# Optimization experiments

Hardware: AMD Instinct MI355X
Metric: run time of the kernel (lower is better)

Reference implementation:

```python
import jax, jax.numpy as jnp
import numpy as np

EMBED_DIM = 512
NUM_HEADS = 8
WINDOW = 64
FFN_RATIO = 4


def _mha(q_in, kv_in, w_in, b_in, w_out, b_out, n_heads, mask=None):
    # Faithful torch.nn.MultiheadAttention (batch_first) with packed in_proj.
    b, sq, d = q_in.shape
    sk = kv_in.shape[1]
    hd = d // n_heads
    wq, wk, wv = jnp.split(w_in, 3, axis=0)   # each [d, d]
    bq, bk, bv = jnp.split(b_in, 3, axis=0)
    q = (q_in @ wq.T + bq).reshape(b, sq, n_heads, hd).transpose(0, 2, 1, 3)
    k = (kv_in @ wk.T + bk).reshape(b, sk, n_heads, hd).transpose(0, 2, 1, 3)
    v = (kv_in @ wv.T + bv).reshape(b, sk, n_heads, hd).transpose(0, 2, 1, 3)
    scores = jnp.einsum('bhqd,bhkd->bhqk', q, k) / jnp.sqrt(jnp.asarray(hd, q.dtype))
    if mask is not None:
        scores = scores + mask  # additive -inf mask, broadcast over [b, h]
    attn = jax.nn.softmax(scores, axis=-1)
    out = jnp.einsum('bhqk,bhkd->bhqd', attn, v)
    out = out.transpose(0, 2, 1, 3).reshape(b, sq, d)
    return out @ w_out.T + b_out


def _layernorm(x, g, b, eps=1e-5):
    mu = jnp.mean(x, axis=-1, keepdims=True)
    var = jnp.var(x, axis=-1, keepdims=True)
    return (x - mu) * jax.lax.rsqrt(var + eps) * g + b


def _local_causal_mask(p, window, dtype=jnp.float32):
    # row i attends to columns [max(0, i-window), i]
    i = jnp.arange(p)[:, None]
    j = jnp.arange(p)[None, :]
    allowed = (j <= i) & (j >= i - window)
    return jnp.where(allowed, jnp.zeros((), dtype), jnp.asarray(-jnp.inf, dtype))


def setup_inputs() -> dict:
    key = jax.random.key(0)
    ks = jax.random.split(key, 20)
    d, h = EMBED_DIM, EMBED_DIM * FFN_RATIO
    s = 0.02
    return {
        'x': jax.random.normal(ks[0], (64, 512, d), jnp.float32),
        'anchors': jax.random.normal(ks[1], (64, 32, d), jnp.float32),
        'lw_in': jax.random.normal(ks[2], (3 * d, d), jnp.float32) * s,
        'lb_in': jnp.zeros((3 * d,), jnp.float32),
        'lw_out': jax.random.normal(ks[3], (d, d), jnp.float32) * s,
        'lb_out': jnp.zeros((d,), jnp.float32),
        'gw_in': jax.random.normal(ks[4], (3 * d, d), jnp.float32) * s,
        'gb_in': jnp.zeros((3 * d,), jnp.float32),
        'gw_out': jax.random.normal(ks[5], (d, d), jnp.float32) * s,
        'gb_out': jnp.zeros((d,), jnp.float32),
        'w1': jax.random.normal(ks[6], (h, d), jnp.float32) * s,
        'b1': jnp.zeros((h,), jnp.float32),
        'w2': jax.random.normal(ks[7], (d, h), jnp.float32) * s,
        'b2': jnp.zeros((d,), jnp.float32),
        'g1': jnp.ones((d,), jnp.float32),
        'be1': jnp.zeros((d,), jnp.float32),
        'g2': jnp.ones((d,), jnp.float32),
        'be2': jnp.zeros((d,), jnp.float32),
    }


def reference(x, anchors, lw_in, lb_in, lw_out, lb_out, gw_in, gb_in, gw_out, gb_out,
              w1, b1, w2, b2, g1, be1, g2, be2):
    p = x.shape[1]
    mask = _local_causal_mask(p, WINDOW, x.dtype)
    x = x + _mha(x, x, lw_in, lb_in, lw_out, lb_out, NUM_HEADS, mask)
    x = x + _mha(x, anchors, gw_in, gb_in, gw_out, gb_out, NUM_HEADS)
    x = _layernorm(x, g1, be1)
    h = jax.nn.gelu(x @ w1.T + b1, approximate=False)
    ffn = h @ w2.T + b2
    return _layernorm(x + ffn, g2, be2)
```

## Files before the change

### kernel.cpp

```cpp
#include <hip/hip_runtime.h>
#include <cmath>


typedef unsigned short u16;
typedef unsigned int u32;
typedef __bf16 bf16_t;
typedef bf16_t bf16x8 __attribute__((ext_vector_type(8)));
typedef float f32x4 __attribute__((ext_vector_type(4)));

#define DEV __device__ __forceinline__
#define MFMA16(a, b, c) __builtin_amdgcn_mfma_f32_16x16x32_bf16(a, b, c, 0, 0, 0)
#define SBAR() __builtin_amdgcn_sched_barrier(0)

DEV u16 f2b(float f) {
  u32 u = __float_as_uint(f);
  u32 r = u + 0x7fffu + ((u >> 16) & 1u);
  return (u16)(r >> 16);
}
DEV float b2f(u16 b) { return __uint_as_float(((u32)b) << 16); }

DEV float gelu_erf(float x) {
  float y = x * 0.70710678118654752f;
  float ay = fabsf(y);
  float t = __builtin_amdgcn_rcpf(1.0f + 0.3275911f * ay);
  float p = t * (0.254829592f +
            t * (-0.284496736f +
            t * (1.421413741f +
            t * (-1.453152027f + t * 1.061405429f))));
  float e = 1.0f - p * __expf(-y * y);
  float erfv = (y < 0.f) ? -e : e;
  return 0.5f * x * (1.0f + erfv);
}

DEV void g2l16(const void* g, void* l) {
  __builtin_amdgcn_global_load_lds((const __attribute__((address_space(1))) void*)g,
                                   (__attribute__((address_space(3))) void*)l,
                                   16, 0, 0);
}

__global__ __launch_bounds__(256) void conv1(const float* __restrict__ s,
                                             u16* __restrict__ d) {
  size_t idx = ((size_t)blockIdx.x * 256 + threadIdx.x) * 8;
  float4 a = *(const float4*)(s + idx);
  float4 b = *(const float4*)(s + idx + 4);
  float v[8] = {a.x, a.y, a.z, a.w, b.x, b.y, b.z, b.w};
  union { u16 q[8]; uint4 u; } pk;
#pragma unroll
  for (int i = 0; i < 8; ++i) pk.q[i] = f2b(v[i]);
  *(uint4*)(d + idx) = pk.u;
}

template <bool GELU, bool RES32, bool RESB, bool LN, bool OUT32, bool OUTB>
__global__ __launch_bounds__(1024, 1) void gemmW(
    const u16* __restrict__ A, const u16* __restrict__ B,
    const float* __restrict__ bias, const float* __restrict__ res32,
    const u16* __restrict__ resb, const float* __restrict__ lnG,
    const float* __restrict__ lnB, float* __restrict__ out32,
    u16* __restrict__ outb, int M, int N, int K) {
  __shared__ __align__(16) char smem[147456];
  const int tid = threadIdx.x;
  const int lane = tid & 63, wv = tid >> 6;
  const int wm = wv >> 3, wn = wv & 7;
  const int lrow = lane & 15, quad = lane >> 4;

  int idx = blockIdx.x;
  {
    const int nwg = gridDim.x;
    if (nwg >= 8) {
      const int q = nwg >> 3, r = nwg & 7;
      const int xcd = idx & 7, rk = idx >> 3;
      idx = (xcd < r ? xcd * (q + 1) : r * (q + 1) + (xcd - r) * q) + rk;
    }
  }
  const int nx = N >> 9;
  const int m0 = (idx / nx) * 128, n0 = (idx % nx) * 512;

  const int c0q = quad ^ (lrow & 3);
  const int hbit = (lrow >> 2) & 1;
  int aOffE[4], aOffO[4], bOff[4];
#pragma unroll
  for (int m = 0; m < 4; ++m) {
    const int rb = (wm * 64 + m * 16 + lrow) * 128;
    aOffE[m] = rb + (c0q + hbit * 4) * 16;
    aOffO[m] = rb + (c0q + (1 - hbit) * 4) * 16;
  }
#pragma unroll
  for (int n = 0; n < 4; ++n)
    bOff[n] = (wn * 64 + n * 16 + lrow) * 64 + ((quad ^ ((lrow >> 1) & 3)) * 16);

  const int lB = (tid & 3) ^ ((tid >> 3) & 3);
  const char* Bsrc0 = (const char*)B + (((size_t)(n0 + (tid >> 2)) * K + lB * 8) << 1);
  const char* Bsrc1 = (const char*)B + (((size_t)(n0 + 256 + (tid >> 2)) * K + lB * 8) << 1);
  const int lA = (tid & 7) ^ ((tid >> 3) & 7);
  const char* Asrc = (const char*)A + (((size_t)(m0 + (tid >> 3)) * K + lA * 8) << 1);

  const int nt = K >> 5, ntp = nt >> 1;
  const int sdst = tid * 16;

  f32x4 acc[4][4];
  f32x4 zero4 = {0.f, 0.f, 0.f, 0.f};
#pragma unroll
  for (int a = 0; a < 4; ++a)
#pragma unroll
    for (int b = 0; b < 4; ++b) acc[a][b] = zero4;

  g2l16(Asrc, smem + sdst);
  g2l16(Asrc + 128, smem + 16384 + sdst);
  g2l16(Bsrc0, smem + 49152 + sdst);
  g2l16(Bsrc1, smem + 49152 + 16384 + sdst);
  g2l16(Bsrc0 + 64, smem + 49152 + 32768 + sdst);
  g2l16(Bsrc1 + 64, smem + 49152 + 32768 + 16384 + sdst);
  SBAR();
  asm volatile("s_waitcnt vmcnt(2)" ::: "memory");
  asm volatile("s_barrier" ::: "memory");
  SBAR();

  int sB0 = 0, sB2 = 2, pA = 0, pA2 = 2;
  for (int tp = 0; tp < ntp; ++tp) {
#pragma unroll
    for (int half = 0; half < 2; ++half) {
      const int t = tp * 2 + half;
      const char* Ab = smem + pA * 16384;
      const char* Bb = smem + 49152 + sB0 * 32768;
      bf16x8 afr[4], bfr[4];
#pragma unroll
      for (int m = 0; m < 4; ++m)
        afr[m] = *(const bf16x8*)(Ab + (half ? aOffO[m] : aOffE[m]));
#pragma unroll
      for (int n = 0; n < 4; ++n)
        bfr[n] = *(const bf16x8*)(Bb + bOff[n]);
      const int ktB = (t + 2 < nt) ? t + 2 : nt - 1;
      char* bd = smem + 49152 + sB2 * 32768;
      g2l16(Bsrc0 + ((size_t)ktB << 6), bd + sdst);
      g2l16(Bsrc1 + ((size_t)ktB << 6), bd + 16384 + sdst);
      if (half == 0) {
        const int p2 = (tp + 2 < ntp) ? tp + 2 : ntp - 1;
        g2l16(Asrc + ((size_t)p2 << 7), smem + pA2 * 16384 + sdst);
      }
      SBAR();
      asm volatile("s_waitcnt lgkmcnt(0)" ::: "memory");
      SBAR();
      __builtin_amdgcn_s_setprio(1);
#pragma unroll
      for (int m = 0; m < 4; ++m)
#pragma unroll
        for (int n = 0; n < 4; ++n)
          acc[m][n] = MFMA16(afr[m], bfr[n], acc[m][n]);
      __builtin_amdgcn_s_setprio(0);
      SBAR();
      asm volatile("s_waitcnt vmcnt(3)" ::: "memory");
      asm volatile("s_barrier" ::: "memory");
      SBAR();
      sB0 = (sB0 == 2) ? 0 : sB0 + 1;
      sB2 = (sB2 == 2) ? 0 : sB2 + 1;
    }
    pA = (pA == 2) ? 0 : pA + 1;
    pA2 = (pA2 == 2) ? 0 : pA2 + 1;
  }

  asm volatile("s_waitcnt vmcnt(0)" ::: "memory");
  __syncthreads();

  float* cw = (float*)(smem + (size_t)wv * 4352);
  float* red = (float*)(smem + 131072);
  const int row16 = lane >> 2;
  const int c0 = (lane & 3) * 16;
  const int gcb = n0 + wn * 64 + c0;
  float bias16[16];
#pragma unroll
  for (int t = 0; t < 4; ++t) {
    float4 b4 = *(const float4*)(bias + gcb + t * 4);
    bias16[t * 4 + 0] = b4.x; bias16[t * 4 + 1] = b4.y;
    bias16[t * 4 + 2] = b4.z; bias16[t * 4 + 3] = b4.w;
  }

  float vv[4][16];
#pragma unroll
  for (int fm = 0; fm < 4; ++fm) {
#pragma unroll
    for (int fn = 0; fn < 4; ++fn)
#pragma unroll
      for (int r = 0; r < 4; ++r)
        cw[(quad * 4 + r) * 68 + fn * 16 + lrow] = acc[fm][fn][r];
    const int grow = m0 + wm * 64 + fm * 16 + row16;
    const size_t gbase = (size_t)grow * N + gcb;
    const float* crp = &cw[row16 * 68 + c0];
    float v[16];
#pragma unroll
    for (int t = 0; t < 4; ++t) {
      f32x4 q = *(const f32x4*)(crp + t * 4);
      v[t * 4 + 0] = q[0] + bias16[t * 4 + 0];
      v[t * 4 + 1] = q[1] + bias16[t * 4 + 1];
      v[t * 4 + 2] = q[2] + bias16[t * 4 + 2];
      v[t * 4 + 3] = q[3] + bias16[t * 4 + 3];
    }
    if (RES32) {
#pragma unroll
      for (int t = 0; t < 4; ++t) {
        float4 rr = *(const float4*)(res32 + gbase + t * 4);
        v[t * 4 + 0] += rr.x; v[t * 4 + 1] += rr.y;
        v[t * 4 + 2] += rr.z; v[t * 4 + 3] += rr.w;
      }
    }
    if (RESB) {
#pragma unroll
      for (int t = 0; t < 2; ++t) {
        union { u16 q[8]; uint4 u; } rb;
        rb.u = *(const uint4*)(resb + gbase + t * 8);
#pragma unroll
        for (int j = 0; j < 8; ++j) v[t * 8 + j] += b2f(rb.q[j]);
      }
    }
    if (GELU) {
#pragma unroll
      for (int e = 0; e < 16; ++e) v[e] = gelu_erf(v[e]);
    }
    if (LN) {
      float s1 = 0.f, s2 = 0.f;
#pragma unroll
      for (int e = 0; e < 16; ++e) { s1 += v[e]; s2 += v[e] * v[e]; }
      s1 += __shfl_xor(s1, 1); s2 += __shfl_xor(s2, 1);
      s1 += __shfl_xor(s1, 2); s2 += __shfl_xor(s2, 2);
      if ((lane & 3) == 0) {
        const int lr = wm * 64 + fm * 16 + row16;
        red[(lr * 8 + wn) * 2 + 0] = s1;
        red[(lr * 8 + wn) * 2 + 1] = s2;
      }
#pragma unroll
      for (int e = 0; e < 16; ++e) vv[fm][e] = v[e];
    } else {
      if (OUT32) {
#pragma unroll
        for (int t = 0; t < 4; ++t) {
          float4 w4 = {v[t * 4 + 0], v[t * 4 + 1], v[t * 4 + 2], v[t * 4 + 3]};
          *(float4*)(out32 + gbase + t * 4) = w4;
        }
      }
      if (OUTB) {
#pragma unroll
        for (int t = 0; t < 2; ++t) {
          union { u16 q[8]; uint4 u; } pk;
#pragma unroll
          for (int j = 0; j < 8; ++j) pk.q[j] = f2b(v[t * 8 + j]);
          *(uint4*)(outb + gbase + t * 8) = pk.u;
        }
      }
    }
  }

  if (LN) {
    __syncthreads();
    float g16[16], b16[16];
#pragma unroll
    for (int t = 0; t < 4; ++t) {
      float4 gg = *(const float4*)(lnG + gcb + t * 4);
      float4 bb = *(const float4*)(lnB + gcb + t * 4);
      g16[t * 4 + 0] = gg.x; g16[t * 4 + 1] = gg.y;
      g16[t * 4 + 2] = gg.z; g16[t * 4 + 3] = gg.w;
      b16[t * 4 + 0] = bb.x; b16[t * 4 + 1] = bb.y;
      b16[t * 4 + 2] = bb.z; b16[t * 4 + 3] = bb.w;
    }
#pragma unroll
    for (int fm = 0; fm < 4; ++fm) {
      const int lr = wm * 64 + fm * 16 + row16;
      const float* rp = &red[lr * 16];
      float s1 = 0.f, s2 = 0.f;
#pragma unroll
      for (int t = 0; t < 4; ++t) {
        f32x4 q = *(const f32x4*)(rp + t * 4);
        s1 += q[0] + q[2];
        s2 += q[1] + q[3];
      }
      const float mean = s1 * (1.0f / 512.0f);
      const float var = s2 * (1.0f / 512.0f) - mean * mean;
      const float rs = rsqrtf(var + 1e-5f);
      const int grow = m0 + wm * 64 + fm * 16 + row16;
      const size_t gbase = (size_t)grow * N + gcb;
      float o[16];
#pragma unroll
      for (int e = 0; e < 16; ++e)
        o[e] = (vv[fm][e] - mean) * rs * g16[e] + b16[e];
      if (OUT32) {
#pragma unroll
        for (int t = 0; t < 4; ++t) {
          float4 w4 = {o[t * 4 + 0], o[t * 4 + 1], o[t * 4 + 2], o[t * 4 + 3]};
          *(float4*)(out32 + gbase + t * 4) = w4;
        }
      }
      if (OUTB) {
#pragma unroll
        for (int t = 0; t < 2; ++t) {
          union { u16 q[8]; uint4 u; } pk;
#pragma unroll
          for (int j = 0; j < 8; ++j) pk.q[j] = f2b(o[t * 8 + j]);
          *(uint4*)(outb + gbase + t * 8) = pk.u;
        }
      }
    }
  }
}

__global__ __launch_bounds__(256) void local_attn_mfma(const u16* __restrict__ qkv,
                                                       u16* __restrict__ outb) {
  __shared__ u16 vt[64][152];
  __shared__ u16 pb[4][16][104];
  const int tid = threadIdx.x;
  const int lane = tid & 63, w = tid >> 6;
  const int c = lane & 15, quad = lane >> 4;
  const int bx = blockIdx.x;
  const int qb = bx & 7, h = (bx >> 3) & 7, bb = bx >> 6;
  const int i0 = qb * 64;
  const int hc = h * 64;
  const size_t rbase = (size_t)bb * 512;

  {
    int r = tid >> 1;
    int d0 = (tid & 1) * 32;
    int key = i0 - 64 + r;
    if (key < 0) key = 0;
    if (key > 511) key = 511;
    const u16* Vr = qkv + (rbase + key) * 1536 + 1024 + hc + d0;
#pragma unroll
    for (int g = 0; g < 4; ++g) {
      union { u16 q[8]; uint4 u; } vv;
      vv.u = *(const uint4*)(Vr + g * 8);
#pragma unroll
      for (int j = 0; j < 8; ++j) vt[d0 + g * 8 + j][r] = vv.q[j];
    }
    if (tid < 128) {
      int r2 = 128 + (tid >> 3);
      int d2 = (tid & 7) * 8;
      int key2 = i0 - 64 + r2;
      if (key2 < 0) key2 = 0;
      if (key2 > 511) key2 = 511;
      const u16* Vr2 = qkv + (rbase + key2) * 1536 + 1024 + hc + d2;
      union { u16 q[8]; uint4 u; } vv2;
      vv2.u = *(const uint4*)Vr2;
#pragma unroll
      for (int j = 0; j < 8; ++j) vt[d2 + j][r2] = vv2.q[j];
    }
  }
  __syncthreads();

  const int i0w = i0 + 16 * w;
  const int kg0 = i0w - 64;

  bf16x8 qf0, qf1;
  {
    const u16* Qr = qkv + (rbase + i0w + c) * 1536 + hc + quad * 8;
    qf0 = *(const bf16x8*)Qr;
    qf1 = *(const bf16x8*)(Qr + 32);
  }

  f32x4 s[5];
#pragma unroll
  for (int kb = 0; kb < 5; ++kb) {
    int key = kg0 + kb * 16 + c; if (key < 0) key = 0;
    const u16* Kr = qkv + (rbase + key) * 1536 + 512 + hc + quad * 8;
    bf16x8 k0 = *(const bf16x8*)Kr;
    bf16x8 k1 = *(const bf16x8*)(Kr + 32);
    f32x4 z = {0.f, 0.f, 0.f, 0.f};
    z = __builtin_amdgcn_mfma_f32_16x16x32_bf16(qf0, k0, z, 0, 0, 0);
    s[kb] = __builtin_amdgcn_mfma_f32_16x16x32_bf16(qf1, k1, z, 0, 0, 0);
  }

  float mx[4];
#pragma unroll
  for (int r = 0; r < 4; ++r) {
    int row = quad * 4 + r;
    float m = -1e30f;
#pragma unroll
    for (int kb = 0; kb < 5; ++kb) {
      float v = s[kb][r] * 0.125f;
      int key = kg0 + kb * 16 + c;
      bool ok = key >= 0;
      if (kb == 0) ok = ok && (c >= row);
      if (kb == 4) ok = ok && (c <= row);
      v = ok ? v : -1e30f;
      s[kb][r] = v;
      m = fmaxf(m, v);
    }
    mx[r] = m;
  }
#pragma unroll
  for (int o = 1; o <= 8; o <<= 1)
#pragma unroll
    for (int r = 0; r < 4; ++r) mx[r] = fmaxf(mx[r], __shfl_xor(mx[r], o));

  float l[4] = {0.f, 0.f, 0.f, 0.f};
#pragma unroll
  for (int kb = 0; kb < 5; ++kb)
#pragma unroll
    for (int r = 0; r < 4; ++r) {
      u16 pq = f2b(__expf(s[kb][r] - mx[r]));
      l[r] += b2f(pq);
      pb[w][quad * 4 + r][kb * 16 + c] = pq;
    }
#pragma unroll
  for (int r = 0; r < 4; ++r) pb[w][quad * 4 + r][80 + c] = 0;
#pragma unroll
  for (int o = 1; o <= 8; o <<= 1)
#pragma unroll
    for (int r = 0; r < 4; ++r) l[r] += __shfl_xor(l[r], o);
  float inv[4];
#pragma unroll
  for (int r = 0; r < 4; ++r) inv[r] = 1.f / l[r];

  f32x4 o4[4];
#pragma unroll
  for (int nb = 0; nb < 4; ++nb) o4[nb] = f32x4{0.f, 0.f, 0.f, 0.f};
#pragma unroll
  for (int kt = 0; kt < 3; ++kt) {
    bf16x8 pa = *(const bf16x8*)&pb[w][c][kt * 32 + quad * 8];
#pragma unroll
    for (int nb = 0; nb < 4; ++nb) {
      bf16x8 vb = *(const bf16x8*)&vt[nb * 16 + c][16 * w + kt * 32 + quad * 8];
      o4[nb] = __builtin_amdgcn_mfma_f32_16x16x32_bf16(pa, vb, o4[nb], 0, 0, 0);
    }
  }
#pragma unroll
  for (int nb = 0; nb < 4; ++nb)
#pragma unroll
    for (int r = 0; r < 4; ++r) {
      int seq = i0w + quad * 4 + r;
      outb[(rbase + seq) * 512 + hc + nb * 16 + c] = f2b(o4[nb][r] * inv[r]);
    }
}

__global__ __launch_bounds__(256) void global_attn_mfma(const u16* __restrict__ qg,
                                                        const u16* __restrict__ kvg,
                                                        u16* __restrict__ outb) {
  __shared__ u16 vt[64][40];
  __shared__ u16 pb[4][16][40];
  const int tid = threadIdx.x;
  const int lane = tid & 63, w = tid >> 6;
  const int c = lane & 15, quad = lane >> 4;
  const int bx = blockIdx.x;
  const int qb = bx & 7, h = (bx >> 3) & 7, bb = bx >> 6;
  const int i0 = qb * 64;
  const int hc = h * 64;
  const size_t rbase = (size_t)bb * 512;

  {
    int r = tid >> 3;
    int d0 = (tid & 7) * 8;
    const u16* Vr = kvg + ((size_t)bb * 32 + r) * 1024 + 512 + hc + d0;
    union { u16 q[8]; uint4 u; } vv;
    vv.u = *(const uint4*)Vr;
#pragma unroll
    for (int j = 0; j < 8; ++j) vt[d0 + j][r] = vv.q[j];
  }
  __syncthreads();

  const int i0w = i0 + 16 * w;
  bf16x8 qf0, qf1;
  {
    const u16* Qr = qg + (rbase + i0w + c) * 512 + hc + quad * 8;
    qf0 = *(const bf16x8*)Qr;
    qf1 = *(const bf16x8*)(Qr + 32);
  }
  f32x4 s[2];
#pragma unroll
  for (int kb = 0; kb < 2; ++kb) {
    const u16* Kr = kvg + ((size_t)bb * 32 + kb * 16 + c) * 1024 + hc + quad * 8;
    bf16x8 k0 = *(const bf16x8*)Kr;
    bf16x8 k1 = *(const bf16x8*)(Kr + 32);
    f32x4 z = {0.f, 0.f, 0.f, 0.f};
    z = __builtin_amdgcn_mfma_f32_16x16x32_bf16(qf0, k0, z, 0, 0, 0);
    s[kb] = __builtin_amdgcn_mfma_f32_16x16x32_bf16(qf1, k1, z, 0, 0, 0);
  }
  float mx[4];
#pragma unroll
  for (int r = 0; r < 4; ++r)
    mx[r] = fmaxf(s[0][r] * 0.125f, s[1][r] * 0.125f);
#pragma unroll
  for (int o = 1; o <= 8; o <<= 1)
#pragma unroll
    for (int r = 0; r < 4; ++r) mx[r] = fmaxf(mx[r], __shfl_xor(mx[r], o));
  float l[4] = {0.f, 0.f, 0.f, 0.f};
#pragma unroll
  for (int kb = 0; kb < 2; ++kb)
#pragma unroll
    for (int r = 0; r < 4; ++r) {
      u16 pq = f2b(__expf(s[kb][r] * 0.125f - mx[r]));
      l[r] += b2f(pq);
      pb[w][quad * 4 + r][kb * 16 + c] = pq;
    }
#pragma unroll
  for (int o = 1; o <= 8; o <<= 1)
#pragma unroll
    for (int r = 0; r < 4; ++r) l[r] += __shfl_xor(l[r], o);
  float inv[4];
#pragma unroll
  for (int r = 0; r < 4; ++r) inv[r] = 1.f / l[r];

  f32x4 o4[4];
#pragma unroll
  for (int nb = 0; nb < 4; ++nb) o4[nb] = f32x4{0.f, 0.f, 0.f, 0.f};
  bf16x8 pa = *(const bf16x8*)&pb[w][c][quad * 8];
#pragma unroll
  for (int nb = 0; nb < 4; ++nb) {
    bf16x8 vb = *(const bf16x8*)&vt[nb * 16 + c][quad * 8];
    o4[nb] = __builtin_amdgcn_mfma_f32_16x16x32_bf16(pa, vb, o4[nb], 0, 0, 0);
  }
#pragma unroll
  for (int nb = 0; nb < 4; ++nb)
#pragma unroll
    for (int r = 0; r < 4; ++r) {
      int seq = i0w + quad * 4 + r;
      outb[(rbase + seq) * 512 + hc + nb * 16 + c] = f2b(o4[nb][r] * inv[r]);
    }
}

extern "C" void kernel_launch(void* const* d_in, const int* in_sizes, int n_in,
                              void* d_out, int out_size, void* d_ws, size_t ws_size,
                              hipStream_t stream) {
  const float* x      = (const float*)d_in[0];
  const float* anchors= (const float*)d_in[1];
  const float* lw_in  = (const float*)d_in[2];
  const float* lb_in  = (const float*)d_in[3];
  const float* lw_out = (const float*)d_in[4];
  const float* lb_out = (const float*)d_in[5];
  const float* gw_in  = (const float*)d_in[6];
  const float* gb_in  = (const float*)d_in[7];
  const float* gw_out = (const float*)d_in[8];
  const float* gb_out = (const float*)d_in[9];
  const float* w1     = (const float*)d_in[10];
  const float* b1     = (const float*)d_in[11];
  const float* w2     = (const float*)d_in[12];
  const float* b2     = (const float*)d_in[13];
  const float* g1     = (const float*)d_in[14];
  const float* be1    = (const float*)d_in[15];
  const float* g2     = (const float*)d_in[16];
  const float* be2    = (const float*)d_in[17];
  (void)in_sizes; (void)n_in; (void)out_size;
  float* out = (float*)d_out;

  char* ws = (char*)d_ws;
  size_t o = 0;
  auto nxt = [&](size_t bytes) { char* p = ws + o; o += bytes; return p; };
  u16* lwib = (u16*)nxt((size_t)1536 * 512 * 2);
  u16* lwob = (u16*)nxt((size_t)512 * 512 * 2);
  u16* gwib = (u16*)nxt((size_t)1536 * 512 * 2);
  u16* gwob = (u16*)nxt((size_t)512 * 512 * 2);
  u16* w1b  = (u16*)nxt((size_t)2048 * 512 * 2);
  u16* w2b  = (u16*)nxt((size_t)512 * 2048 * 2);
  u16* ab   = (u16*)nxt((size_t)2048 * 512 * 2);
  u16* kvgb = (u16*)nxt((size_t)2048 * 1024 * 2);
  const size_t wbytes = o;

  int nc = 1;
  while (wbytes + (size_t)(32768 / nc) * 6144 > ws_size && nc < 32) nc <<= 1;
  const int Mc = 32768 / nc;
  const int nBat = Mc / 512;
  const int mbW = Mc >> 7;
  u16* BIGb = (u16*)nxt((size_t)Mc * 4096);
  u16* Pb   = (u16*)nxt((size_t)Mc * 1024);
  u16* Qb   = (u16*)nxt((size_t)Mc * 1024);
  u16* Sb   = BIGb + (size_t)Mc * 1536;

  conv1<<<384, 256, 0, stream>>>(lw_in, lwib);
  conv1<<<128, 256, 0, stream>>>(lw_out, lwob);
  conv1<<<384, 256, 0, stream>>>(gw_in, gwib);
  conv1<<<128, 256, 0, stream>>>(gw_out, gwob);
  conv1<<<512, 256, 0, stream>>>(w1, w1b);
  conv1<<<512, 256, 0, stream>>>(w2, w2b);
  conv1<<<512, 256, 0, stream>>>(anchors, ab);
  gemmW<false, false, false, false, false, true><<<16 * 2, 1024, 0, stream>>>(
      ab, gwib + 512 * 512, gb_in + 512, nullptr, nullptr, nullptr, nullptr,
      nullptr, kvgb, 2048, 1024, 512);

  for (int ck = 0; ck < nc; ++ck) {
    const size_t r0 = (size_t)ck * Mc;
    const float* xck = x + r0 * 512;
    conv1<<<Mc / 4, 256, 0, stream>>>(xck, Pb);
    gemmW<false, false, false, false, false, true><<<mbW * 3, 1024, 0, stream>>>(
        Pb, lwib, lb_in, nullptr, nullptr, nullptr, nullptr,
        nullptr, BIGb, Mc, 1536, 512);
    local_attn_mfma<<<nBat * 64, 256, 0, stream>>>(BIGb, Sb);
    gemmW<false, true, false, false, false, true><<<mbW, 1024, 0, stream>>>(
        Sb, lwob, lb_out, xck, nullptr, nullptr, nullptr,
        nullptr, Qb, Mc, 512, 512);
    gemmW<false, false, false, false, false, true><<<mbW, 1024, 0, stream>>>(
        Qb, gwib, gb_in, nullptr, nullptr, nullptr, nullptr,
        nullptr, Pb, Mc, 512, 512);
    global_attn_mfma<<<nBat * 64, 256, 0, stream>>>(Pb, kvgb + (r0 / 512) * 32 * 1024, Sb);
    gemmW<false, false, true, true, false, true><<<mbW, 1024, 0, stream>>>(
        Sb, gwob, gb_out, nullptr, Qb, g1, be1,
        nullptr, Qb, Mc, 512, 512);
    gemmW<true, false, false, false, false, true><<<mbW * 4, 1024, 0, stream>>>(
        Qb, w1b, b1, nullptr, nullptr, nullptr, nullptr,
        nullptr, BIGb, Mc, 2048, 512);
    gemmW<false, false, true, true, true, false><<<mbW, 1024, 0, stream>>>(
        BIGb, w2b, b2, nullptr, Qb, g2, be2,
        out + r0 * 512, nullptr, Mc, 512, 2048);
  }
}
```

Baseline: 615.7 us.

## Halve GEMM block to 512 threads with 64x128 warp tiles

```diff
diff --git a/kernel.cpp b/kernel.cpp
--- a/kernel.cpp
+++ b/kernel.cpp
@@ -51,7 +51,7 @@
 }
 
 template <bool GELU, bool RES32, bool RESB, bool LN, bool OUT32, bool OUTB>
-__global__ __launch_bounds__(1024, 1) void gemmW(
+__global__ __launch_bounds__(512, 2) void gemmV(
     const u16* __restrict__ A, const u16* __restrict__ B,
     const float* __restrict__ bias, const float* __restrict__ res32,
     const u16* __restrict__ resb, const float* __restrict__ lnG,
@@ -60,7 +60,7 @@
   __shared__ __align__(16) char smem[147456];
   const int tid = threadIdx.x;
   const int lane = tid & 63, wv = tid >> 6;
-  const int wm = wv >> 3, wn = wv & 7;
+  const int wm = wv >> 2, wn = wv & 3;
   const int lrow = lane & 15, quad = lane >> 4;
 
   int idx = blockIdx.x;
@@ -77,7 +77,7 @@
 
   const int c0q = quad ^ (lrow & 3);
   const int hbit = (lrow >> 2) & 1;
-  int aOffE[4], aOffO[4], bOff[4];
+  int aOffE[4], aOffO[4], bOff[8];
 #pragma unroll
   for (int m = 0; m < 4; ++m) {
     const int rb = (wm * 64 + m * 16 + lrow) * 128;
@@ -85,33 +85,43 @@
     aOffO[m] = rb + (c0q + (1 - hbit) * 4) * 16;
   }
 #pragma unroll
-  for (int n = 0; n < 4; ++n)
-    bOff[n] = (wn * 64 + n * 16 + lrow) * 64 + ((quad ^ ((lrow >> 1) & 3)) * 16);
+  for (int n = 0; n < 8; ++n)
+    bOff[n] = (wn * 128 + n * 16 + lrow) * 64 + ((quad ^ ((lrow >> 1) & 3)) * 16);
 
   const int lB = (tid & 3) ^ ((tid >> 3) & 3);
-  const char* Bsrc0 = (const char*)B + (((size_t)(n0 + (tid >> 2)) * K + lB * 8) << 1);
-  const char* Bsrc1 = (const char*)B + (((size_t)(n0 + 256 + (tid >> 2)) * K + lB * 8) << 1);
   const int lA = (tid & 7) ^ ((tid >> 3) & 7);
-  const char* Asrc = (const char*)A + (((size_t)(m0 + (tid >> 3)) * K + lA * 8) << 1);
+  const char* BsrcT = (const char*)B + (((size_t)(n0 + (tid >> 2)) * K + lB * 8) << 1);
+  const size_t bRow128 = ((size_t)K << 1) * 128;
+  const char* Asrc0 = (const char*)A + (((size_t)(m0 + (tid >> 3)) * K + lA * 8) << 1);
+  const char* Asrc1 = Asrc0 + (((size_t)K << 1) * 64);
+  const int sdst = tid * 16;
 
   const int nt = K >> 5, ntp = nt >> 1;
-  const int sdst = tid * 16;
-
-  f32x4 acc[4][4];
+
+  auto stageB = [&](int kt, int slot) {
+    const char* g = BsrcT + ((size_t)kt << 6);
+    char* d = smem + 49152 + slot * 32768 + sdst;
+#pragma unroll
+    for (int r = 0; r < 4; ++r) g2l16(g + r * bRow128, d + r * 8192);
+  };
+  auto stageA = [&](int pr, int hf, int slot) {
+    g2l16((hf ? Asrc1 : Asrc0) + ((size_t)pr << 7),
+          smem + slot * 16384 + hf * 8192 + sdst);
+  };
+
+  f32x4 acc[4][8];
   f32x4 zero4 = {0.f, 0.f, 0.f, 0.f};
 #pragma unroll
   for (int a = 0; a < 4; ++a)
 #pragma unroll
-    for (int b = 0; b < 4; ++b) acc[a][b] = zero4;
-
-  g2l16(Asrc, smem + sdst);
-  g2l16(Asrc + 128, smem + 16384 + sdst);
-  g2l16(Bsrc0, smem + 49152 + sdst);
-  g2l16(Bsrc1, smem + 49152 + 16384 + sdst);
-  g2l16(Bsrc0 + 64, smem + 49152 + 32768 + sdst);
-  g2l16(Bsrc1 + 64, smem + 49152 + 32768 + 16384 + sdst);
+    for (int b = 0; b < 8; ++b) acc[a][b] = zero4;
+
+  stageA(0, 0, 0); stageA(0, 1, 0);
+  stageB(0, 0);
+  stageB(1, 1);
+  stageA(1, 0, 1); stageA(1, 1, 1);
   SBAR();
-  asm volatile("s_waitcnt vmcnt(2)" ::: "memory");
+  asm volatile("s_waitcnt vmcnt(6)" ::: "memory");
   asm volatile("s_barrier" ::: "memory");
   SBAR();
 
@@ -122,21 +132,17 @@
       const int t = tp * 2 + half;
       const char* Ab = smem + pA * 16384;
       const char* Bb = smem + 49152 + sB0 * 32768;
-      bf16x8 afr[4], bfr[4];
+      bf16x8 afr[4], bfr[8];
 #pragma unroll
       for (int m = 0; m < 4; ++m)
         afr[m] = *(const bf16x8*)(Ab + (half ? aOffO[m] : aOffE[m]));
 #pragma unroll
-      for (int n = 0; n < 4; ++n)
+      for (int n = 0; n < 8; ++n)
         bfr[n] = *(const bf16x8*)(Bb + bOff[n]);
       const int ktB = (t + 2 < nt) ? t + 2 : nt - 1;
-      char* bd = smem + 49152 + sB2 * 32768;
-      g2l16(Bsrc0 + ((size_t)ktB << 6), bd + sdst);
-      g2l16(Bsrc1 + ((size_t)ktB << 6), bd + 16384 + sdst);
-      if (half == 0) {
-        const int p2 = (tp + 2 < ntp) ? tp + 2 : ntp - 1;
-        g2l16(Asrc + ((size_t)p2 << 7), smem + pA2 * 16384 + sdst);
-      }
+      stageB(ktB, sB2);
+      const int p2 = (tp + 2 < ntp) ? tp + 2 : ntp - 1;
+      stageA(p2, half, pA2);
       SBAR();
       asm volatile("s_waitcnt lgkmcnt(0)" ::: "memory");
       SBAR();
@@ -144,11 +150,11 @@
 #pragma unroll
       for (int m = 0; m < 4; ++m)
 #pragma unroll
-        for (int n = 0; n < 4; ++n)
+        for (int n = 0; n < 8; ++n)
           acc[m][n] = MFMA16(afr[m], bfr[n], acc[m][n]);
       __builtin_amdgcn_s_setprio(0);
       SBAR();
-      asm volatile("s_waitcnt vmcnt(3)" ::: "memory");
+      asm volatile("s_waitcnt vmcnt(5)" ::: "memory");
       asm volatile("s_barrier" ::: "memory");
       SBAR();
       sB0 = (sB0 == 2) ? 0 : sB0 + 1;
@@ -165,135 +171,125 @@
   float* red = (float*)(smem + 131072);
   const int row16 = lane >> 2;
   const int c0 = (lane & 3) * 16;
-  const int gcb = n0 + wn * 64 + c0;
-  float bias16[16];
-#pragma unroll
-  for (int t = 0; t < 4; ++t) {
-    float4 b4 = *(const float4*)(bias + gcb + t * 4);
-    bias16[t * 4 + 0] = b4.x; bias16[t * 4 + 1] = b4.y;
-    bias16[t * 4 + 2] = b4.z; bias16[t * 4 + 3] = b4.w;
-  }
-
-  float vv[4][16];
+
 #pragma unroll
   for (int fm = 0; fm < 4; ++fm) {
-#pragma unroll
-    for (int fn = 0; fn < 4; ++fn)
-#pragma unroll
-      for (int r = 0; r < 4; ++r)
-        cw[(quad * 4 + r) * 68 + fn * 16 + lrow] = acc[fm][fn][r];
     const int grow = m0 + wm * 64 + fm * 16 + row16;
-    const size_t gbase = (size_t)grow * N + gcb;
-    const float* crp = &cw[row16 * 68 + c0];
-    float v[16];
-#pragma unroll
-    for (int t = 0; t < 4; ++t) {
-      f32x4 q = *(const f32x4*)(crp + t * 4);
-      v[t * 4 + 0] = q[0] + bias16[t * 4 + 0];
-      v[t * 4 + 1] = q[1] + bias16[t * 4 + 1];
-      v[t * 4 + 2] = q[2] + bias16[t * 4 + 2];
-      v[t * 4 + 3] = q[3] + bias16[t * 4 + 3];
-    }
-    if (RES32) {
+    float vv[2][16];
+    float s1 = 0.f, s2 = 0.f;
+#pragma unroll
+    for (int hf = 0; hf < 2; ++hf) {
+#pragma unroll
+      for (int fn = 0; fn < 4; ++fn)
+#pragma unroll
+        for (int r = 0; r < 4; ++r)
+          cw[(quad * 4 + r) * 68 + fn * 16 + lrow] = acc[fm][hf * 4 + fn][r];
+      const int gcb = n0 + wn * 128 + hf * 64 + c0;
+      const size_t gbase = (size_t)grow * N + gcb;
+      const float* crp = &cw[row16 * 68 + c0];
+      float v[16];
 #pragma unroll
       for (int t = 0; t < 4; ++t) {
-        float4 rr = *(const float4*)(res32 + gbase + t * 4);
-        v[t * 4 + 0] += rr.x; v[t * 4 + 1] += rr.y;
-        v[t * 4 + 2] += rr.z; v[t * 4 + 3] += rr.w;
-      }
-    }
-    if (RESB) {
-#pragma unroll
-      for (int t = 0; t < 2; ++t) {
-        union { u16 q[8]; uint4 u; } rb;
-        rb.u = *(const uint4*)(resb + gbase + t * 8);
-#pragma unroll
-        for (int j = 0; j < 8; ++j) v[t * 8 + j] += b2f(rb.q[j]);
-      }
-    }
-    if (GELU) {
-#pragma unroll
-      for (int e = 0; e < 16; ++e) v[e] = gelu_erf(v[e]);
+        f32x4 q = *(const f32x4*)(crp + t * 4);
+        float4 b4 = *(const float4*)(bias + gcb + t * 4);
+        v[t * 4 + 0] = q[0] + b4.x;
+        v[t * 4 + 1] = q[1] + b4.y;
+        v[t * 4 + 2] = q[2] + b4.z;
+        v[t * 4 + 3] = q[3] + b4.w;
+      }
+      if (RES32) {
+#pragma unroll
+        for (int t = 0; t < 4; ++t) {
+          float4 rr = *(const float4*)(res32 + gbase + t * 4);
+          v[t * 4 + 0] += rr.x; v[t * 4 + 1] += rr.y;
+          v[t * 4 + 2] += rr.z; v[t * 4 + 3] += rr.w;
+        }
+      }
+      if (RESB) {
+#pragma unroll
+        for (int t = 0; t < 2; ++t) {
+          union { u16 q[8]; uint4 u; } rb;
+          rb.u = *(const uint4*)(resb + gbase + t * 8);
+#pragma unroll
+          for (int j = 0; j < 8; ++j) v[t * 8 + j] += b2f(rb.q[j]);
+        }
+      }
+      if (GELU) {
+#pragma unroll
+        for (int e = 0; e < 16; ++e) v[e] = gelu_erf(v[e]);
+      }
+      if (LN) {
+#pragma unroll
+        for (int e = 0; e < 16; ++e) {
+          s1 += v[e];
+          s2 += v[e] * v[e];
+          vv[hf][e] = v[e];
+        }
+      } else {
+        if (OUT32) {
+#pragma unroll
+          for (int t = 0; t < 4; ++t) {
+            float4 w4 = {v[t * 4 + 0], v[t * 4 + 1], v[t * 4 + 2], v[t * 4 + 3]};
+            *(float4*)(out32 + gbase + t * 4) = w4;
+          }
+        }
+        if (OUTB) {
+#pragma unroll
+          for (int t = 0; t < 2; ++t) {
+            union { u16 q[8]; uint4 u; } pk;
+#pragma unroll
+            for (int j = 0; j < 8; ++j) pk.q[j] = f2b(v[t * 8 + j]);
+            *(uint4*)(outb + gbase + t * 8) = pk.u;
+          }
+        }
+      }
     }
     if (LN) {
-      float s1 = 0.f, s2 = 0.f;
-#pragma unroll
-      for (int e = 0; e < 16; ++e) { s1 += v[e]; s2 += v[e] * v[e]; }
       s1 += __shfl_xor(s1, 1); s2 += __shfl_xor(s2, 1);
       s1 += __shfl_xor(s1, 2); s2 += __shfl_xor(s2, 2);
+      const int lr = wm * 64 + fm * 16 + row16;
       if ((lane & 3) == 0) {
-        const int lr = wm * 64 + fm * 16 + row16;
-        red[(lr * 8 + wn) * 2 + 0] = s1;
-        red[(lr * 8 + wn) * 2 + 1] = s2;
-      }
-#pragma unroll
-      for (int e = 0; e < 16; ++e) vv[fm][e] = v[e];
-    } else {
-      if (OUT32) {
+        red[lr * 8 + wn * 2 + 0] = s1;
+        red[lr * 8 + wn * 2 + 1] = s2;
+      }
+      __syncthreads();
+      const float* rp = &red[lr * 8];
+      f32x4 qa = *(const f32x4*)rp;
+      f32x4 qb = *(const f32x4*)(rp + 4);
+      const float t1 = qa[0] + qa[2] + qb[0] + qb[2];
+      const float t2 = qa[1] + qa[3] + qb[1] + qb[3];
+      const float mean = t1 * (1.0f / 512.0f);
+      const float var = t2 * (1.0f / 512.0f) - mean * mean;
+      const float rs = rsqrtf(var + 1e-5f);
+#pragma unroll
+      for (int hf = 0; hf < 2; ++hf) {
+        const int gcb = n0 + wn * 128 + hf * 64 + c0;
+        const size_t gbase = (size_t)grow * N + gcb;
+        float o[16];
 #pragma unroll
         for (int t = 0; t < 4; ++t) {
-          float4 w4 = {v[t * 4 + 0], v[t * 4 + 1], v[t * 4 + 2], v[t * 4 + 3]};
-          *(float4*)(out32 + gbase + t * 4) = w4;
-        }
-      }
-      if (OUTB) {
-#pragma unroll
-        for (int t = 0; t < 2; ++t) {
-          union { u16 q[8]; uint4 u; } pk;
-#pragma unroll
-          for (int j = 0; j < 8; ++j) pk.q[j] = f2b(v[t * 8 + j]);
-          *(uint4*)(outb + gbase + t * 8) = pk.u;
-        }
-      }
-    }
-  }
-
-  if (LN) {
-    __syncthreads();
-    float g16[16], b16[16];
-#pragma unroll
-    for (int t = 0; t < 4; ++t) {
-      float4 gg = *(const float4*)(lnG + gcb + t * 4);
-      float4 bb = *(const float4*)(lnB + gcb + t * 4);
-      g16[t * 4 + 0] = gg.x; g16[t * 4 + 1] = gg.y;
-      g16[t * 4 + 2] = gg.z; g16[t * 4 + 3] = gg.w;
-      b16[t * 4 + 0] = bb.x; b16[t * 4 + 1] = bb.y;
-      b16[t * 4 + 2] = bb.z; b16[t * 4 + 3] = bb.w;
-    }
-#pragma unroll
-    for (int fm = 0; fm < 4; ++fm) {
-      const int lr = wm * 64 + fm * 16 + row16;
-      const float* rp = &red[lr * 16];
-      float s1 = 0.f, s2 = 0.f;
-#pragma unroll
-      for (int t = 0; t < 4; ++t) {
-        f32x4 q = *(const f32x4*)(rp + t * 4);
-        s1 += q[0] + q[2];
-        s2 += q[1] + q[3];
-      }
-      const float mean = s1 * (1.0f / 512.0f);
-      const float var = s2 * (1.0f / 512.0f) - mean * mean;
-      const float rs = rsqrtf(var + 1e-5f);
-      const int grow = m0 + wm * 64 + fm * 16 + row16;
-      const size_t gbase = (size_t)grow * N + gcb;
-      float o[16];
-#pragma unroll
-      for (int e = 0; e < 16; ++e)
-        o[e] = (vv[fm][e] - mean) * rs * g16[e] + b16[e];
-      if (OUT32) {
-#pragma unroll
-        for (int t = 0; t < 4; ++t) {
-          float4 w4 = {o[t * 4 + 0], o[t * 4 + 1], o[t * 4 + 2], o[t * 4 + 3]};
-          *(float4*)(out32 + gbase + t * 4) = w4;
-        }
-      }
-      if (OUTB) {
-#pragma unroll
-        for (int t = 0; t < 2; ++t) {
-          union { u16 q[8]; uint4 u; } pk;
-#pragma unroll
-          for (int j = 0; j < 8; ++j) pk.q[j] = f2b(o[t * 8 + j]);
-          *(uint4*)(outb + gbase + t * 8) = pk.u;
+          float4 gg = *(const float4*)(lnG + gcb + t * 4);
+          float4 bb = *(const float4*)(lnB + gcb + t * 4);
+          o[t * 4 + 0] = (vv[hf][t * 4 + 0] - mean) * rs * gg.x + bb.x;
+          o[t * 4 + 1] = (vv[hf][t * 4 + 1] - mean) * rs * gg.y + bb.y;
+          o[t * 4 + 2] = (vv[hf][t * 4 + 2] - mean) * rs * gg.z + bb.z;
+          o[t * 4 + 3] = (vv[hf][t * 4 + 3] - mean) * rs * gg.w + bb.w;
+        }
+        if (OUT32) {
+#pragma unroll
+          for (int t = 0; t < 4; ++t) {
+            float4 w4 = {o[t * 4 + 0], o[t * 4 + 1], o[t * 4 + 2], o[t * 4 + 3]};
+            *(float4*)(out32 + gbase + t * 4) = w4;
+          }
+        }
+        if (OUTB) {
+#pragma unroll
+          for (int t = 0; t < 2; ++t) {
+            union { u16 q[8]; uint4 u; } pk;
+#pragma unroll
+            for (int j = 0; j < 8; ++j) pk.q[j] = f2b(o[t * 8 + j]);
+            *(uint4*)(outb + gbase + t * 8) = pk.u;
+          }
         }
       }
     }
@@ -566,7 +562,7 @@
   conv1<<<512, 256, 0, stream>>>(w1, w1b);
   conv1<<<512, 256, 0, stream>>>(w2, w2b);
   conv1<<<512, 256, 0, stream>>>(anchors, ab);
-  gemmW<false, false, false, false, false, true><<<16 * 2, 1024, 0, stream>>>(
+  gemmV<false, false, false, false, false, true><<<16 * 2, 512, 0, stream>>>(
       ab, gwib + 512 * 512, gb_in + 512, nullptr, nullptr, nullptr, nullptr,
       nullptr, kvgb, 2048, 1024, 512);
 
@@ -574,24 +570,24 @@
     const size_t r0 = (size_t)ck * Mc;
     const float* xck = x + r0 * 512;
     conv1<<<Mc / 4, 256, 0, stream>>>(xck, Pb);
-    gemmW<false, false, false, false, false, true><<<mbW * 3, 1024, 0, stream>>>(
+    gemmV<false, false, false, false, false, true><<<mbW * 3, 512, 0, stream>>>(
         Pb, lwib, lb_in, nullptr, nullptr, nullptr, nullptr,
         nullptr, BIGb, Mc, 1536, 512);
     local_attn_mfma<<<nBat * 64, 256, 0, stream>>>(BIGb, Sb);
-    gemmW<false, true, false, false, false, true><<<mbW, 1024, 0, stream>>>(
+    gemmV<false, true, false, false, false, true><<<mbW, 512, 0, stream>>>(
         Sb, lwob, lb_out, xck, nullptr, nullptr, nullptr,
         nullptr, Qb, Mc, 512, 512);
-    gemmW<false, false, false, false, false, true><<<mbW, 1024, 0, stream>>>(
+    gemmV<false, false, false, false, false, true><<<mbW, 512, 0, stream>>>(
         Qb, gwib, gb_in, nullptr, nullptr, nullptr, nullptr,
         nullptr, Pb, Mc, 512, 512);
     global_attn_mfma<<<nBat * 64, 256, 0, stream>>>(Pb, kvgb + (r0 / 512) * 32 * 1024, Sb);
-    gemmW<false, false, true, true, false, true><<<mbW, 1024, 0, stream>>>(
+    gemmV<false, false, true, true, false, true><<<mbW, 512, 0, stream>>>(
         Sb, gwob, gb_out, nullptr, Qb, g1, be1,
         nullptr, Qb, Mc, 512, 512);
-    gemmW<true, false, false, false, false, true><<<mbW * 4, 1024, 0, stream>>>(
+    gemmV<true, false, false, false, false, true><<<mbW * 4, 512, 0, stream>>>(
         Qb, w1b, b1, nullptr, nullptr, nullptr, nullptr,
         nullptr, BIGb, Mc, 2048, 512);
-    gemmW<false, false, true, true, true, false><<<mbW, 1024, 0, stream>>>(
+    gemmV<false, false, true, true, true, false><<<mbW, 512, 0, stream>>>(
         BIGb, w2b, b2, nullptr, Qb, g2, be2,
         out + r0 * 512, nullptr, Mc, 512, 2048);
   }
```

Measured after the change: 625.9 us. About the same (+1.7%).
